# Optimization experiments

Measured on AMD Instinct MI355X. Metric: run time of the kernel, lower is better.

Reference implementation:

```python
import jax, jax.numpy as jnp
import numpy as np
import math

B, T, D = 1, 4096, 1024
H = 16
HD = D // H  # 64


def _rotate_half(x):
    d = x.shape[-1] // 2
    return jnp.concatenate([-x[..., d:], x[..., :d]], axis=-1)


def setup_inputs() -> dict:
    key = jax.random.key(0)
    k1, k2, k3 = jax.random.split(key, 3)
    x = jax.random.normal(k1, (B, T, D), dtype=jnp.float32)
    # Linear weights stored as (in, out) so forward is x @ W
    w_qkv = jax.random.normal(k2, (D, 3 * D), dtype=jnp.float32) * (1.0 / math.sqrt(D))
    w_proj = jax.random.normal(k3, (D, D), dtype=jnp.float32) * (1.0 / math.sqrt(D))
    return {"x": x, "w_qkv": w_qkv, "w_proj": w_proj}


def reference(x, w_qkv, w_proj):
    b, t, c = x.shape
    qkv = x @ w_qkv  # [b,t,3c]
    q, k, v = jnp.split(qkv, 3, axis=-1)
    # [b,h,t,hd]
    q = q.reshape(b, t, H, HD).transpose(0, 2, 1, 3)
    k = k.reshape(b, t, H, HD).transpose(0, 2, 1, 3)
    v = v.reshape(b, t, H, HD).transpose(0, 2, 1, 3)

    # RoPE (rotate_half style)
    inv_freq = 1.0 / (10000.0 ** (jnp.arange(0, HD, 2, dtype=jnp.float32) / HD))
    pos = jnp.arange(t, dtype=jnp.float32)
    freqs = jnp.outer(pos, inv_freq)            # [t, hd/2]
    cos = jnp.concatenate([jnp.cos(freqs), jnp.cos(freqs)], axis=-1)[None, None]  # [1,1,t,hd]
    sin = jnp.concatenate([jnp.sin(freqs), jnp.sin(freqs)], axis=-1)[None, None]
    q = q * cos + _rotate_half(q) * sin
    k = k * cos + _rotate_half(k) * sin

    att = jnp.einsum('bhqd,bhkd->bhqk', q, k) / math.sqrt(HD)  # [b,h,t,t]
    causal = jnp.tril(jnp.ones((t, t), dtype=bool))
    att = jnp.where(causal, att, -jnp.inf)
    att = jax.nn.softmax(att, axis=-1)
    # dropout is identity in eval mode
    y = jnp.einsum('bhqk,bhkd->bhqd', att, v)
    y = y.transpose(0, 2, 1, 3).reshape(b, t, c)
    return y @ w_proj
```

## Files before the change

kernel.cpp:

```cpp
#include <hip/hip_runtime.h>
#include <hip/hip_fp16.h>
#include <math.h>

#define TT 4096
#define DD 1024
#define NH 16
#define HD 64

typedef __attribute__((ext_vector_type(8))) _Float16 half8v;
typedef __attribute__((ext_vector_type(4))) _Float16 half4v;
typedef __attribute__((ext_vector_type(4))) float f32x4;

#define GLDS16(g, l)                                                        \
    __builtin_amdgcn_global_load_lds(                                       \
        (const __attribute__((address_space(1))) void*)(g),                 \
        (__attribute__((address_space(3))) void*)(l), 16, 0, 0)

__global__ __launch_bounds__(256) void cast_x_zero(
    const float* __restrict__ X, _Float16* __restrict__ Xh,
    float4* __restrict__ O4, float4* __restrict__ L4)
{
    const int t = blockIdx.x * 256 + threadIdx.x;
    const int i = t * 8;
    float4 a = *(const float4*)&X[i];
    float4 b = *(const float4*)&X[i + 4];
    half8v o = {(_Float16)a.x, (_Float16)a.y, (_Float16)a.z, (_Float16)a.w,
                (_Float16)b.x, (_Float16)b.y, (_Float16)b.z, (_Float16)b.w};
    *(half8v*)&Xh[i] = o;
    const float4 z = {0.f, 0.f, 0.f, 0.f};
    O4[t] = z;
    if (t < 16384) L4[t] = z;
}

__global__ __launch_bounds__(256) void transpose_cast(
    const float* __restrict__ W, _Float16* __restrict__ WT, int K, int N)
{
    __shared__ float tile[64][65];
    const int t = threadIdx.x;
    const int k0 = blockIdx.y * 64, n0 = blockIdx.x * 64;
    const int c = (t & 15) * 4, r = t >> 4;
#pragma unroll
    for (int i = 0; i < 4; i++) {
        float4 v = *(const float4*)&W[(size_t)(k0 + r + 16 * i) * N + n0 + c];
        tile[r + 16 * i][c + 0] = v.x;
        tile[r + 16 * i][c + 1] = v.y;
        tile[r + 16 * i][c + 2] = v.z;
        tile[r + 16 * i][c + 3] = v.w;
    }
    __syncthreads();
#pragma unroll
    for (int i = 0; i < 4; i++) {
        const int n = r + 16 * i;
        half4v o;
        o[0] = (_Float16)tile[c + 0][n];
        o[1] = (_Float16)tile[c + 1][n];
        o[2] = (_Float16)tile[c + 2][n];
        o[3] = (_Float16)tile[c + 3][n];
        *(half4v*)&WT[(size_t)(n0 + n) * K + k0 + c] = o;
    }
}

template <int MODE>
__global__ __launch_bounds__(256) void gemm_h(
    const _Float16* __restrict__ A, const _Float16* __restrict__ Bt,
    float* __restrict__ C0, _Float16* __restrict__ Q,
    _Float16* __restrict__ Kk, _Float16* __restrict__ V,
    int M, int N, int K)
{
    __shared__ _Float16 As[128 * 32];
    __shared__ _Float16 Bs[128 * 32];
    const int tid  = threadIdx.x;
    const int wave = tid >> 6;
    const int lane = tid & 63;
    const int quad = lane >> 4;
    const int n16  = lane & 15;
    const int n0 = blockIdx.x * 128;
    const int m0 = blockIdx.y * 128;
    const int wr = (wave & 1) * 64;
    const int wc = (wave >> 1) * 64;

    f32x4 acc[4][4];
#pragma unroll
    for (int i = 0; i < 4; i++)
#pragma unroll
        for (int j = 0; j < 4; j++) acc[i][j] = (f32x4){0.f, 0.f, 0.f, 0.f};

    const int srow = tid >> 2;
    const int schk = tid & 3;
    const int sswz = (schk ^ ((srow >> 1) & 3)) * 8;
    const _Float16* Ag = A + (size_t)(m0 + srow) * K + sswz;
    const _Float16* Bg = Bt + (size_t)(n0 + srow) * K + sswz;
    _Float16* AsW = As + (size_t)wave * 512;
    _Float16* BsW = Bs + (size_t)wave * 512;
    const int slot = (quad ^ ((n16 >> 1) & 3)) * 8;

    for (int k0 = 0; k0 < K; k0 += 32) {
        __syncthreads();
        GLDS16(Ag + k0, AsW);
        GLDS16(Ag + (size_t)64 * K + k0, AsW + 2048);
        GLDS16(Bg + k0, BsW);
        GLDS16(Bg + (size_t)64 * K + k0, BsW + 2048);
        __syncthreads();

        half8v aF[4], bF[4];
#pragma unroll
        for (int i = 0; i < 4; i++)
            aF[i] = *(const half8v*)&As[(size_t)(wr + i * 16 + n16) * 32 + slot];
#pragma unroll
        for (int j = 0; j < 4; j++)
            bF[j] = *(const half8v*)&Bs[(size_t)(wc + j * 16 + n16) * 32 + slot];
#pragma unroll
        for (int i = 0; i < 4; i++)
#pragma unroll
            for (int j = 0; j < 4; j++)
                acc[i][j] = __builtin_amdgcn_mfma_f32_16x16x32_f16(
                    aF[i], bF[j], acc[i][j], 0, 0, 0);
    }

    if (MODE == 0) {
#pragma unroll
        for (int i = 0; i < 4; i++)
#pragma unroll
            for (int j = 0; j < 4; j++)
#pragma unroll
                for (int r = 0; r < 4; r++) {
                    const int m = m0 + wr + i * 16 + quad * 4 + r;
                    const int n = n0 + wc + j * 16 + n16;
                    C0[(size_t)m * N + n] = acc[i][j][r];
                }
    } else {
        const int ncol0 = n0 + wc;
        const int which = ncol0 >> 10;
        const int h = (ncol0 & 1023) >> 6;
        if (which < 2) {
            _Float16* dst = (which == 0) ? Q : Kk;
            const float sc = (which == 0) ? 0.125f * 1.44269504f : 1.0f;
            const float K2 = 0.4152410118609203f;
#pragma unroll
            for (int jlo = 0; jlo < 2; jlo++) {
                const int d = jlo * 16 + n16;
                const float invf = exp2f(-(float)d * K2);
#pragma unroll
                for (int i = 0; i < 4; i++) {
#pragma unroll
                    for (int r = 0; r < 4; r++) {
                        const int t = m0 + wr + i * 16 + quad * 4 + r;
                        const float f = (float)t * invf;
                        float sn, cs;
                        __sincosf(f, &sn, &cs);
                        const float lo = acc[i][jlo][r];
                        const float hi = acc[i][jlo + 2][r];
                        const size_t off = ((size_t)h * TT + t) * HD + d;
                        dst[off]      = (_Float16)((lo * cs - hi * sn) * sc);
                        dst[off + 32] = (_Float16)((hi * cs + lo * sn) * sc);
                    }
                }
            }
        } else {
#pragma unroll
            for (int kb2 = 0; kb2 < 2; kb2++) {
                const int kbg = ((m0 + wr) >> 5) + kb2;
#pragma unroll
                for (int j = 0; j < 4; j++) {
                    const int d = j * 16 + n16;
                    half8v o;
#pragma unroll
                    for (int r = 0; r < 4; r++) {
                        o[2 * r]     = (_Float16)acc[2 * kb2][j][r];
                        o[2 * r + 1] = (_Float16)acc[2 * kb2 + 1][j][r];
                    }
                    *(half8v*)(V + (((size_t)h * (TT / 32) + kbg) * 64 + d) * 32
                               + quad * 8) = o;
                }
            }
        }
    }
}

__global__ __launch_bounds__(256) void attn_kernel(
    const _Float16* __restrict__ Qh, const _Float16* __restrict__ Kh,
    const _Float16* __restrict__ Vp, _Float16* __restrict__ Oacc,
    float* __restrict__ Lacc)
{
    __shared__ _Float16 Ks[2][32][32];
    __shared__ _Float16 Vs[64][32];
    __shared__ _Float16 Ps[4][32][40];

    const int tid  = threadIdx.x;
    const int wave = tid >> 6;
    const int lane = tid & 63;
    const int quad = lane >> 4;
    const int n16  = lane & 15;
    const int h  = blockIdx.z;
    const int qt = 31 - blockIdx.y;
    const int s  = blockIdx.x;
    const int nT = 4 * qt + 4;
    const int nS = (qt + 8) >> 3;
    if (s >= nS) return;
    const int t_beg = s * nT / nS;
    const int t_end = (s + 1) * nT / nS;

    const int q0 = qt * 128;
    const int rowbase = q0 + wave * 32;

    const _Float16* Qg = Qh + (size_t)h * TT * HD;
    const _Float16* Kg = Kh + (size_t)h * TT * HD;
    const _Float16* Vg = Vp + (size_t)h * (TT / 32) * 2048;

    half8v aQ[2][2];
#pragma unroll
    for (int g = 0; g < 2; g++) {
        const int row = rowbase + g * 16 + n16;
#pragma unroll
        for (int c = 0; c < 2; c++)
            aQ[g][c] = *(const half8v*)(Qg + (size_t)row * HD + c * 32 + quad * 8);
    }

    f32x4 O[2][4], Ol[2];
#pragma unroll
    for (int g = 0; g < 2; g++) {
#pragma unroll
        for (int d = 0; d < 4; d++) O[g][d] = (f32x4){0.f, 0.f, 0.f, 0.f};
        Ol[g] = (f32x4){0.f, 0.f, 0.f, 0.f};
    }
    const half8v vOnes = {(_Float16)1, (_Float16)1, (_Float16)1, (_Float16)1,
                          (_Float16)1, (_Float16)1, (_Float16)1, (_Float16)1};

    const int kc = tid >> 7, kj = (tid >> 2) & 31, ks = tid & 3;
    const _Float16* kSrc = Kg + (size_t)kj * HD + kc * 32
                           + (size_t)(ks ^ ((kj >> 1) & 3)) * 8;
    const int vd = tid >> 2, vs = tid & 3;
    const _Float16* vSrc = Vg + (size_t)vd * 32
                           + (size_t)(vs ^ ((vd >> 1) & 3)) * 8;
    _Float16* ksBase = &Ks[0][0][0] + (size_t)wave * 512;
    _Float16* vsBase = &Vs[0][0] + (size_t)wave * 512;
    const int slot = (quad ^ ((n16 >> 1) & 3)) * 8;

    for (int it = t_beg; it < t_end; ++it) {
        const int j0 = it * 32;
        __syncthreads();
        GLDS16(kSrc + (size_t)j0 * HD, ksBase);
        GLDS16(vSrc + (size_t)it * 2048, vsBase);
        __syncthreads();

        if (j0 <= rowbase + 31) {
            const bool needMask = (j0 + 31 > rowbase);

            f32x4 S[2][2];
#pragma unroll
            for (int g = 0; g < 2; g++)
#pragma unroll
                for (int st = 0; st < 2; st++) {
                    S[g][st] = (f32x4){0.f, 0.f, 0.f, 0.f};
#pragma unroll
                    for (int c = 0; c < 2; c++) {
                        half8v bK = *(const half8v*)&Ks[c][st * 16 + n16][slot];
                        S[g][st] = __builtin_amdgcn_mfma_f32_16x16x32_f16(
                            aQ[g][c], bK, S[g][st], 0, 0, 0);
                    }
                }

#pragma unroll
            for (int g = 0; g < 2; g++)
#pragma unroll
                for (int r = 0; r < 4; r++) {
                    const int row = rowbase + g * 16 + quad * 4 + r;
                    float x0 = S[g][0][r];
                    float x1 = S[g][1][r];
                    if (needMask) {
                        x0 = (j0 + n16      <= row) ? x0 : -1e30f;
                        x1 = (j0 + 16 + n16 <= row) ? x1 : -1e30f;
                    }
                    const float p0 = __builtin_amdgcn_exp2f(x0);
                    const float p1 = __builtin_amdgcn_exp2f(x1);
                    *(__half2*)&Ps[wave][g * 16 + quad * 4 + r][2 * n16] =
                        __floats2half2_rn(p0, p1);
                }

            half8v bV[4];
#pragma unroll
            for (int d = 0; d < 4; d++)
                bV[d] = *(const half8v*)&Vs[d * 16 + n16][slot];
#pragma unroll
            for (int g = 0; g < 2; g++) {
                half8v aP = *(const half8v*)&Ps[wave][g * 16 + n16][quad * 8];
#pragma unroll
                for (int d = 0; d < 4; d++)
                    O[g][d] = __builtin_amdgcn_mfma_f32_16x16x32_f16(
                        aP, bV[d], O[g][d], 0, 0, 0);
                Ol[g] = __builtin_amdgcn_mfma_f32_16x16x32_f16(
                    aP, vOnes, Ol[g], 0, 0, 0);
            }
        }
    }

#pragma unroll
    for (int g = 0; g < 2; g++)
#pragma unroll
        for (int r = 0; r < 4; r++) {
            const int row = rowbase + g * 16 + quad * 4 + r;
            if (n16 == 0)
                unsafeAtomicAdd(&Lacc[h * TT + row], Ol[g][r]);
#pragma unroll
            for (int d = 0; d < 4; d++) {
                float v = O[g][d][r];
                float vn = __shfl_xor(v, 1);
                if ((lane & 1) == 0) {
                    __half2* dst = (__half2*)(Oacc +
                        ((size_t)h * TT + row) * HD + d * 16 + n16);
                    unsafeAtomicAdd(dst, __floats2half2_rn(v, vn));
                }
            }
        }
}

__global__ __launch_bounds__(256) void finalize(
    const _Float16* __restrict__ Oacc, const float* __restrict__ Lacc,
    _Float16* __restrict__ Y)
{
    const int gid = blockIdx.x * 256 + threadIdx.x;
    const int h = gid >> 15;
    const int rem = gid & 32767;
    const int t = rem >> 3;
    const int c = rem & 7;
    const float inv = 1.0f / Lacc[h * TT + t];
    half8v o = *(const half8v*)(Oacc + ((size_t)h * TT + t) * HD + c * 8);
    half8v y;
#pragma unroll
    for (int e = 0; e < 8; e++) y[e] = (_Float16)((float)o[e] * inv);
    *(half8v*)(Y + (size_t)t * DD + h * HD + c * 8) = y;
}

extern "C" void kernel_launch(void* const* d_in, const int* in_sizes, int n_in,
                              void* d_out, int out_size, void* d_ws, size_t ws_size,
                              hipStream_t stream)
{
    const float* x      = (const float*)d_in[0];
    const float* w_qkv  = (const float*)d_in[1];
    const float* w_proj = (const float*)d_in[2];
    float* out = (float*)d_out;

    char* ws = (char*)d_ws;
    const size_t MB = 1u << 20;
    _Float16* xh   = (_Float16*)(ws);
    _Float16* WqT  = (_Float16*)(ws + 8 * MB);
    _Float16* WpT  = (_Float16*)(ws + 14 * MB);
    _Float16* Qh   = (_Float16*)(ws + 16 * MB);
    _Float16* Kh   = (_Float16*)(ws + 24 * MB);
    _Float16* Vp   = (_Float16*)(ws + 32 * MB);
    _Float16* Yh   = (_Float16*)(ws + 40 * MB);
    _Float16* Oacc = (_Float16*)(ws + 48 * MB);
    float*    Lacc = (float*)(ws + 57 * MB);

    dim3 blk(256);

    cast_x_zero<<<2048, blk, 0, stream>>>(x, xh, (float4*)Oacc, (float4*)Lacc);
    transpose_cast<<<dim3(3072 / 64, DD / 64), blk, 0, stream>>>(w_qkv, WqT, DD, 3 * DD);
    transpose_cast<<<dim3(DD / 64, DD / 64), blk, 0, stream>>>(w_proj, WpT, DD, DD);

    gemm_h<1><<<dim3(3072 / 128, TT / 128), blk, 0, stream>>>(
        xh, WqT, nullptr, Qh, Kh, Vp, TT, 3 * DD, DD);

    attn_kernel<<<dim3(4, 32, NH), blk, 0, stream>>>(Qh, Kh, Vp, Oacc, Lacc);

    finalize<<<2048, blk, 0, stream>>>(Oacc, Lacc, Yh);

    gemm_h<0><<<dim3(DD / 128, TT / 128), blk, 0, stream>>>(
        Yh, WpT, out, nullptr, nullptr, nullptr, TT, DD, DD);
}
```

Baseline: 263.6 us.

## Load K/V directly into registers per wave, prefetch K, drop LDS barriers

The attention loop no longer stages K and V tiles through shared memory with two block-wide barriers per 32-key step. Each wave now reads its K fragments straight from global memory into registers, double-buffering them so the next tile's K load overlaps the current tile's work. V fragments are read directly from the pre-packed layout. Each wave also caps its loop at its own causal limit and returns early when it has no work. The cost is that each of the four waves fetches the same K/V data separately, relying on cache, and the V loads are not prefetched.

```diff
diff --git a/kernel.cpp b/kernel.cpp
--- a/kernel.cpp
+++ b/kernel.cpp
@@ -182,8 +182,6 @@
     const _Float16* __restrict__ Vp, _Float16* __restrict__ Oacc,
     float* __restrict__ Lacc)
 {
-    __shared__ _Float16 Ks[2][32][32];
-    __shared__ _Float16 Vs[64][32];
     __shared__ _Float16 Ps[4][32][40];
 
     const int tid  = threadIdx.x;
@@ -202,10 +200,13 @@
 
     const int q0 = qt * 128;
     const int rowbase = q0 + wave * 32;
+    const int t_lim = (rowbase + 31) / 32 + 1;
+    const int t_end_w = t_end < t_lim ? t_end : t_lim;
+    if (t_beg >= t_end_w) return;
 
     const _Float16* Qg = Qh + (size_t)h * TT * HD;
-    const _Float16* Kg = Kh + (size_t)h * TT * HD;
-    const _Float16* Vg = Vp + (size_t)h * (TT / 32) * 2048;
+    const _Float16* Kb0 = Kh + (size_t)h * TT * HD + (size_t)n16 * HD + quad * 8;
+    const _Float16* Vb0 = Vp + (size_t)h * (TT / 32) * 2048 + n16 * 32 + quad * 8;
 
     half8v aQ[2][2];
 #pragma unroll
@@ -226,72 +227,73 @@
     const half8v vOnes = {(_Float16)1, (_Float16)1, (_Float16)1, (_Float16)1,
                           (_Float16)1, (_Float16)1, (_Float16)1, (_Float16)1};
 
-    const int kc = tid >> 7, kj = (tid >> 2) & 31, ks = tid & 3;
-    const _Float16* kSrc = Kg + (size_t)kj * HD + kc * 32
-                           + (size_t)(ks ^ ((kj >> 1) & 3)) * 8;
-    const int vd = tid >> 2, vs = tid & 3;
-    const _Float16* vSrc = Vg + (size_t)vd * 32
-                           + (size_t)(vs ^ ((vd >> 1) & 3)) * 8;
-    _Float16* ksBase = &Ks[0][0][0] + (size_t)wave * 512;
-    _Float16* vsBase = &Vs[0][0] + (size_t)wave * 512;
-    const int slot = (quad ^ ((n16 >> 1) & 3)) * 8;
-
-    for (int it = t_beg; it < t_end; ++it) {
-        const int j0 = it * 32;
-        __syncthreads();
-        GLDS16(kSrc + (size_t)j0 * HD, ksBase);
-        GLDS16(vSrc + (size_t)it * 2048, vsBase);
-        __syncthreads();
-
-        if (j0 <= rowbase + 31) {
-            const bool needMask = (j0 + 31 > rowbase);
-
-            f32x4 S[2][2];
-#pragma unroll
-            for (int g = 0; g < 2; g++)
-#pragma unroll
-                for (int st = 0; st < 2; st++) {
-                    S[g][st] = (f32x4){0.f, 0.f, 0.f, 0.f};
-#pragma unroll
-                    for (int c = 0; c < 2; c++) {
-                        half8v bK = *(const half8v*)&Ks[c][st * 16 + n16][slot];
-                        S[g][st] = __builtin_amdgcn_mfma_f32_16x16x32_f16(
-                            aQ[g][c], bK, S[g][st], 0, 0, 0);
-                    }
-                }
-
-#pragma unroll
-            for (int g = 0; g < 2; g++)
-#pragma unroll
-                for (int r = 0; r < 4; r++) {
-                    const int row = rowbase + g * 16 + quad * 4 + r;
-                    float x0 = S[g][0][r];
-                    float x1 = S[g][1][r];
-                    if (needMask) {
-                        x0 = (j0 + n16      <= row) ? x0 : -1e30f;
-                        x1 = (j0 + 16 + n16 <= row) ? x1 : -1e30f;
-                    }
-                    const float p0 = __builtin_amdgcn_exp2f(x0);
-                    const float p1 = __builtin_amdgcn_exp2f(x1);
-                    *(__half2*)&Ps[wave][g * 16 + quad * 4 + r][2 * n16] =
-                        __floats2half2_rn(p0, p1);
-                }
-
-            half8v bV[4];
-#pragma unroll
-            for (int d = 0; d < 4; d++)
-                bV[d] = *(const half8v*)&Vs[d * 16 + n16][slot];
-#pragma unroll
-            for (int g = 0; g < 2; g++) {
-                half8v aP = *(const half8v*)&Ps[wave][g * 16 + n16][quad * 8];
-#pragma unroll
-                for (int d = 0; d < 4; d++)
-                    O[g][d] = __builtin_amdgcn_mfma_f32_16x16x32_f16(
-                        aP, bV[d], O[g][d], 0, 0, 0);
-                Ol[g] = __builtin_amdgcn_mfma_f32_16x16x32_f16(
-                    aP, vOnes, Ol[g], 0, 0, 0);
-            }
-        }
+#define LOADK(dst, itx)                                                      \
+    do {                                                                     \
+        const _Float16* _p = Kb0 + (size_t)(itx) * 2048;                     \
+        dst[0] = *(const half8v*)(_p);                                       \
+        dst[1] = *(const half8v*)(_p + 32);                                  \
+        dst[2] = *(const half8v*)(_p + 1024);                                \
+        dst[3] = *(const half8v*)(_p + 1056);                                \
+    } while (0)
+
+#define PROCESS(kc, kn, itx)                                                 \
+    do {                                                                     \
+        const int j0 = (itx) * 32;                                           \
+        half8v bV[4];                                                        \
+        _Pragma("unroll")                                                    \
+        for (int d = 0; d < 4; d++)                                          \
+            bV[d] = *(const half8v*)(Vb0 + (size_t)(itx) * 2048 + d * 512);  \
+        f32x4 S[2][2];                                                       \
+        _Pragma("unroll")                                                    \
+        for (int g = 0; g < 2; g++)                                          \
+            _Pragma("unroll")                                                \
+            for (int st = 0; st < 2; st++) {                                 \
+                S[g][st] = (f32x4){0.f, 0.f, 0.f, 0.f};                      \
+                S[g][st] = __builtin_amdgcn_mfma_f32_16x16x32_f16(           \
+                    aQ[g][0], kc[st * 2], S[g][st], 0, 0, 0);                \
+                S[g][st] = __builtin_amdgcn_mfma_f32_16x16x32_f16(           \
+                    aQ[g][1], kc[st * 2 + 1], S[g][st], 0, 0, 0);            \
+            }                                                                \
+        if ((itx) + 1 < t_end_w) LOADK(kn, (itx) + 1);                       \
+        const bool needMask = (j0 + 31 > rowbase);                           \
+        _Pragma("unroll")                                                    \
+        for (int g = 0; g < 2; g++)                                          \
+            _Pragma("unroll")                                                \
+            for (int r = 0; r < 4; r++) {                                    \
+                const int row = rowbase + g * 16 + quad * 4 + r;             \
+                float x0 = S[g][0][r];                                       \
+                float x1 = S[g][1][r];                                       \
+                if (needMask) {                                              \
+                    x0 = (j0 + n16      <= row) ? x0 : -1e30f;               \
+                    x1 = (j0 + 16 + n16 <= row) ? x1 : -1e30f;               \
+                }                                                            \
+                const float p0 = __builtin_amdgcn_exp2f(x0);                 \
+                const float p1 = __builtin_amdgcn_exp2f(x1);                 \
+                *(__half2*)&Ps[wave][g * 16 + quad * 4 + r][2 * n16] =       \
+                    __floats2half2_rn(p0, p1);                               \
+            }                                                                \
+        _Pragma("unroll")                                                    \
+        for (int g = 0; g < 2; g++) {                                        \
+            half8v aP = *(const half8v*)&Ps[wave][g * 16 + n16][quad * 8];   \
+            _Pragma("unroll")                                                \
+            for (int d = 0; d < 4; d++)                                      \
+                O[g][d] = __builtin_amdgcn_mfma_f32_16x16x32_f16(            \
+                    aP, bV[d], O[g][d], 0, 0, 0);                            \
+            Ol[g] = __builtin_amdgcn_mfma_f32_16x16x32_f16(                  \
+                aP, vOnes, Ol[g], 0, 0, 0);                                  \
+        }                                                                    \
+    } while (0)
+
+    half8v kA[4], kB[4];
+    LOADK(kA, t_beg);
+    int it = t_beg;
+    for (;;) {
+        PROCESS(kA, kB, it);
+        ++it;
+        if (it >= t_end_w) break;
+        PROCESS(kB, kA, it);
+        ++it;
+        if (it >= t_end_w) break;
     }
 
 #pragma unroll
```

Result: slower. 337.7 us (+28.1%).
